# Optimization experiments

Measured on AMD Instinct MI355X. Metric: run time of the kernel, lower is better.

## Reference

```python
import jax, jax.numpy as jnp
import numpy as np

B, N, NH, E = 4, 4096, 16, 64
MD, FF, H, PE = 128, 256, 4, 32
DH = MD // H
SCALE = 1.0 / np.float32(np.sqrt(DH))


def _ln(x, g, b, eps=1e-5):
    m = jnp.mean(x, axis=-1, keepdims=True)
    v = jnp.var(x, axis=-1, keepdims=True)
    return (x - m) * jax.lax.rsqrt(v + eps) * g + b


def setup_inputs() -> dict:
    key = jax.random.key(0)
    ks = jax.random.split(key, 16)
    rn = lambda k, shape: jax.random.normal(k, shape, dtype=jnp.float32) * 0.02
    return {
        "x": jax.random.normal(ks[0], (B, N, NH, E), dtype=jnp.float32),
        "pos1": jax.random.normal(ks[1], (B, N, NH, NH), dtype=jnp.float32),
        "pos2": jax.random.normal(ks[2], (B, N, NH, NH), dtype=jnp.float32),
        # input_mlp: Linear(E->MD, no bias) + LayerNorm
        "W_in": rn(ks[3], (E, MD)), "g_in": jnp.ones((MD,), jnp.float32), "b_in": jnp.zeros((MD,), jnp.float32),
        # pos_embedder (simple MLP on stacked rel-coords) + emb_proj_bias (PE->H, no bias)
        "W_pe": rn(ks[4], (2, PE)),
        "W_bias": rn(ks[5], (PE, H)),
        # MHA qkv projections (with bias) and output projection
        "Wq": rn(ks[6], (MD, MD)), "bq": jnp.zeros((MD,), jnp.float32),
        "Wk": rn(ks[7], (MD, MD)), "bk": jnp.zeros((MD,), jnp.float32),
        "Wv": rn(ks[8], (MD, MD)), "bv": jnp.zeros((MD,), jnp.float32),
        "Wo": rn(ks[9], (MD, MD)), "bo": jnp.zeros((MD,), jnp.float32),
        # mlp_layer: Linear(MD->FF,no bias), SiLU, Linear(FF->MD,no bias)
        "W1": rn(ks[10], (MD, FF)), "W2": rn(ks[11], (FF, MD)),
        "g1": jnp.ones((MD,), jnp.float32), "b1": jnp.zeros((MD,), jnp.float32),
        "g2": jnp.ones((MD,), jnp.float32), "b2": jnp.zeros((MD,), jnp.float32),
    }


def reference(x, pos1, pos2, W_in, g_in, b_in, W_pe, W_bias,
              Wq, bq, Wk, bk, Wv, bv, Wo, bo, W1, W2, g1, b1, g2, b2):
    b, n, nh, _ = x.shape
    # input_mlp
    h = _ln(x @ W_in, g_in, b_in)                      # [b,n,nh,MD]
    t = h.reshape(b * n, nh, MD)                       # windows of nh tokens
    # relative-position bias: pos_embedder then emb_proj_bias
    pe = jax.nn.silu(jnp.stack([pos1, pos2], axis=-1).reshape(b * n, nh, nh, 2) @ W_pe)  # [bn,nh,nh,PE]
    bias = pe @ W_bias                                  # [bn,nh,nh,H]
    # MHA with additive bias
    q = (t @ Wq + bq).reshape(b * n, nh, H, DH)
    k = (t @ Wk + bk).reshape(b * n, nh, H, DH)
    v = (t @ Wv + bv).reshape(b * n, nh, H, DH)
    scores = jnp.einsum('bqhd,bkhd->bhqk', q, k) * SCALE + jnp.transpose(bias, (0, 3, 1, 2))
    att = jax.nn.softmax(scores, axis=-1)               # [bn,H,nh,nh]
    o = jnp.einsum('bhqk,bkhd->bqhd', att, v).reshape(b * n, nh, MD)
    att_out = o @ Wo + bo
    # residual (q_res=True, dropout=0) + norms + FFN
    y = _ln(t + att_out, g1, b1)
    y = _ln(y + jax.nn.silu(y @ W1) @ W2, g2, b2)
    return y.reshape(b, n, nh, MD)
```

## Files before the change

### kernel.cpp

```cpp
#include <hip/hip_runtime.h>
#include <hip/hip_bf16.h>
#include <math.h>

#define NHT 16
#define MD 128
#define FFD 256
#define NHEAD 4
#define DH 32
#define PED 32
#define ED 64
#define SCALE 0.17677669529663687f
#define SCB 136
#define SCU 40

typedef __attribute__((ext_vector_type(8))) short bf8;
typedef __attribute__((ext_vector_type(4))) float f32x4;
union U8 { bf8 v; unsigned short s[8]; uint u[4]; uint4 q; };

#define MFMA __builtin_amdgcn_mfma_f32_16x16x32_bf16

__device__ __forceinline__ unsigned short bf1(float a){
  __hip_bfloat16 h = __float2bfloat16(a);
  return *reinterpret_cast<unsigned short*>(&h);
}
__device__ __forceinline__ float bfh2f(unsigned short s){
  __hip_bfloat16 h = *reinterpret_cast<__hip_bfloat16*>(&s);
  return __bfloat162float(h);
}
__device__ __forceinline__ float silu_f(float x){ return x / (1.f + __expf(-x)); }

__device__ __forceinline__ void lnC(float (&C)[8][4], const float* __restrict__ g,
                                    const float* __restrict__ b, int lm){
#pragma unroll
  for (int r = 0; r < 4; ++r){
    float s = 0.f, ss = 0.f;
#pragma unroll
    for (int nt = 0; nt < 8; ++nt){ s += C[nt][r]; ss = fmaf(C[nt][r], C[nt][r], ss); }
#pragma unroll
    for (int m = 1; m < 16; m <<= 1){ s += __shfl_xor(s, m); ss += __shfl_xor(ss, m); }
    float mean = s * (1.f/128.f);
    float var  = ss * (1.f/128.f) - mean*mean;
    float rs   = rsqrtf(var + 1e-5f);
#pragma unroll
    for (int nt = 0; nt < 8; ++nt)
      C[nt][r] = fmaf((C[nt][r] - mean) * rs, g[nt*16+lm], b[nt*16+lm]);
  }
}

__global__ __launch_bounds__(256)
void packw(const float* __restrict__ Wq, const float* __restrict__ Wk,
           const float* __restrict__ Wv, const float* __restrict__ Wo,
           const float* __restrict__ W1, const float* __restrict__ W2,
           uint4* __restrict__ ws){
  int id = blockIdx.x * 256 + threadIdx.x;
  const float* W; int KT, N, u; uint4* dst;
  if      (id < 2048) { W = Wq;  KT = 4; N = 128; dst = ws;         u = id;         }
  else if (id < 4096) { W = Wk;  KT = 4; N = 128; dst = ws + 2048;  u = id - 2048;  }
  else if (id < 6144) { W = Wv;  KT = 4; N = 128; dst = ws + 4096;  u = id - 4096;  }
  else if (id < 8192) { W = Wo;  KT = 4; N = 128; dst = ws + 6144;  u = id - 6144;  }
  else if (id < 12288){ W = W1;  KT = 4; N = 256; dst = ws + 8192;  u = id - 8192;  }
  else                { W = W2;  KT = 8; N = 128; dst = ws + 12288; u = id - 12288; }
  int lane = u & 63, tile = u >> 6;
  int kt = tile % KT, nt = tile / KT;
  int kr  = kt*32 + ((lane >> 4) << 3);
  int col = nt*16 + (lane & 15);
  const float* p = W + (size_t)kr * N + col;
  U8 hi;
#pragma unroll
  for (int j = 0; j < 8; ++j) hi.s[j] = bf1(p[(size_t)j * N]);
  dst[u] = hi.q;
}

__global__ __launch_bounds__(64)
void nha_mfma(const float* __restrict__ x, const float* __restrict__ pos1,
              const float* __restrict__ pos2,
              const float* __restrict__ W_in,
              const float* __restrict__ g_in, const float* __restrict__ b_in,
              const float* __restrict__ W_pe, const float* __restrict__ W_bias,
              const float* __restrict__ bq, const float* __restrict__ bk,
              const float* __restrict__ bv, const float* __restrict__ bo,
              const float* __restrict__ g1, const float* __restrict__ b1,
              const float* __restrict__ g2, const float* __restrict__ b2,
              const uint4* __restrict__ wsp, float* __restrict__ out)
{
  const uint4* pWq  = wsp;
  const uint4* pWk  = wsp + 2048;
  const uint4* pWv  = wsp + 4096;
  const uint4* pWo  = wsp + 6144;
  const uint4* pW1  = wsp + 8192;
  const uint4* pW2  = wsp + 12288;

  __shared__ __align__(16) unsigned short Qb[NHT*SCB];
  __shared__ __align__(16) unsigned short Kb[NHT*SCB];
  __shared__ __align__(16) unsigned short Vb[NHT*SCB];
  __shared__ __align__(16) unsigned short Tb[NHT*SCB];
  __shared__ __align__(16) unsigned short Ub[NHT*SCU];
  __shared__ __align__(16) float Bsm[NHEAD*NHT*NHT];

  const int tid = threadIdx.x;
  const int wi  = blockIdx.x;
  const int lm  = tid & 15;
  const int lg  = tid >> 4;
  const f32x4 zero4 = {0.f,0.f,0.f,0.f};

  bf8 xA[2];
  {
    const float* xp = x + (size_t)wi*1024 + lm*ED + lg*8;
#pragma unroll
    for (int kt = 0; kt < 2; ++kt){
      U8 h;
#pragma unroll
      for (int j = 0; j < 8; ++j) h.s[j] = bf1(xp[kt*32 + j]);
      xA[kt] = h.v;
    }
  }
  float tC[8][4];
#pragma unroll
  for (int nt = 0; nt < 8; ++nt){
    f32x4 acc = zero4;
#pragma unroll
    for (int kt = 0; kt < 2; ++kt){
      const float* wp = W_in + (size_t)(kt*32 + lg*8)*MD + nt*16 + lm;
      U8 w;
#pragma unroll
      for (int j = 0; j < 8; ++j) w.s[j] = bf1(wp[(size_t)j*MD]);
      acc = MFMA(xA[kt], w.v, acc, 0,0,0);
    }
#pragma unroll
    for (int r = 0; r < 4; ++r) tC[nt][r] = acc[r];
  }
  lnC(tC, g_in, b_in, lm);

#pragma unroll
  for (int nt = 0; nt < 8; ++nt)
#pragma unroll
    for (int r = 0; r < 4; ++r)
      Tb[(lg*4+r)*SCB + nt*16+lm] = bf1(tC[nt][r]);
  __syncthreads();
  bf8 tA[4];
#pragma unroll
  for (int kt = 0; kt < 4; ++kt)
    tA[kt] = *(const bf8*)(Tb + lm*SCB + kt*32 + lg*8);
  __syncthreads();

#pragma unroll
  for (int nt = 0; nt < 8; ++nt){
    float bb = bq[nt*16+lm];
    f32x4 acc = {bb,bb,bb,bb};
#pragma unroll
    for (int kt = 0; kt < 4; ++kt){
      U8 bh; bh.q = pWq[(nt*4+kt)*64 + tid];
      acc = MFMA(tA[kt], bh.v, acc, 0,0,0);
    }
#pragma unroll
    for (int r = 0; r < 4; ++r) Qb[(lg*4+r)*SCB + nt*16+lm] = bf1(acc[r]);
  }
#pragma unroll
  for (int nt = 0; nt < 8; ++nt){
    float bb = bk[nt*16+lm];
    f32x4 acc = {bb,bb,bb,bb};
#pragma unroll
    for (int kt = 0; kt < 4; ++kt){
      U8 bh; bh.q = pWk[(nt*4+kt)*64 + tid];
      acc = MFMA(tA[kt], bh.v, acc, 0,0,0);
    }
#pragma unroll
    for (int r = 0; r < 4; ++r) Kb[(lg*4+r)*SCB + nt*16+lm] = bf1(acc[r]);
  }
#pragma unroll
  for (int nt = 0; nt < 8; ++nt){
    float bb = bv[nt*16+lm];
    f32x4 acc = {bb,bb,bb,bb};
#pragma unroll
    for (int kt = 0; kt < 4; ++kt){
      U8 bh; bh.q = pWv[(nt*4+kt)*64 + tid];
      acc = MFMA(tA[kt], bh.v, acc, 0,0,0);
    }
#pragma unroll
    for (int r = 0; r < 4; ++r) Vb[(lg*4+r)*SCB + nt*16+lm] = bf1(acc[r]);
  }

  for (int p = tid; p < NHT*NHT; p += 64){
    float p1 = pos1[(size_t)wi*256 + p];
    float p2 = pos2[(size_t)wi*256 + p];
    float a0=0.f, a1=0.f, a2=0.f, a3=0.f;
#pragma unroll
    for (int i = 0; i < PED; ++i){
      float e = fmaf(p1, W_pe[i], p2 * W_pe[PED+i]);
      float sv = silu_f(e);
      a0 = fmaf(sv, W_bias[i*4+0], a0);
      a1 = fmaf(sv, W_bias[i*4+1], a1);
      a2 = fmaf(sv, W_bias[i*4+2], a2);
      a3 = fmaf(sv, W_bias[i*4+3], a3);
    }
    Bsm[0*256 + p] = a0; Bsm[1*256 + p] = a1; Bsm[2*256 + p] = a2; Bsm[3*256 + p] = a3;
  }
  __syncthreads();

  {
    const int h  = tid >> 4;
    const int qi = tid & 15;
    float qf[DH];
    {
      const unsigned short* qp = Qb + qi*SCB + h*DH;
#pragma unroll
      for (int d0 = 0; d0 < DH; d0 += 8){
        U8 u; u.v = *(const bf8*)(qp + d0);
#pragma unroll
        for (int j = 0; j < 8; ++j) qf[d0+j] = bfh2f(u.s[j]);
      }
    }
    float sc[NHT];
#pragma unroll
    for (int ki = 0; ki < NHT; ++ki){
      const unsigned short* kp = Kb + ki*SCB + h*DH;
      float dot = 0.f;
#pragma unroll
      for (int d0 = 0; d0 < DH; d0 += 8){
        U8 u; u.v = *(const bf8*)(kp + d0);
#pragma unroll
        for (int j = 0; j < 8; ++j) dot = fmaf(qf[d0+j], bfh2f(u.s[j]), dot);
      }
      sc[ki] = fmaf(dot, SCALE, Bsm[h*256 + qi*16 + ki]);
    }
    float mx = sc[0];
#pragma unroll
    for (int ki = 1; ki < NHT; ++ki) mx = fmaxf(mx, sc[ki]);
    float sum = 0.f;
#pragma unroll
    for (int ki = 0; ki < NHT; ++ki){ sc[ki] = __expf(sc[ki]-mx); sum += sc[ki]; }
    const float inv = 1.f/sum;
    float of[DH];
#pragma unroll
    for (int d = 0; d < DH; ++d) of[d] = 0.f;
#pragma unroll
    for (int ki = 0; ki < NHT; ++ki){
      const unsigned short* vp = Vb + ki*SCB + h*DH;
      const float a = sc[ki];
#pragma unroll
      for (int d0 = 0; d0 < DH; d0 += 8){
        U8 u; u.v = *(const bf8*)(vp + d0);
#pragma unroll
        for (int j = 0; j < 8; ++j) of[d0+j] = fmaf(a, bfh2f(u.s[j]), of[d0+j]);
      }
    }
    unsigned short* op_ = Qb + qi*SCB + h*DH;
#pragma unroll
    for (int d = 0; d < DH; ++d) op_[d] = bf1(of[d]*inv);
  }
  __syncthreads();

  bf8 oA[4];
#pragma unroll
  for (int kt = 0; kt < 4; ++kt)
    oA[kt] = *(const bf8*)(Qb + lm*SCB + kt*32 + lg*8);
#pragma unroll
  for (int nt = 0; nt < 8; ++nt){
    float bb = bo[nt*16+lm];
    f32x4 acc = {bb,bb,bb,bb};
#pragma unroll
    for (int kt = 0; kt < 4; ++kt){
      U8 bh; bh.q = pWo[(nt*4+kt)*64 + tid];
      acc = MFMA(oA[kt], bh.v, acc, 0,0,0);
    }
#pragma unroll
    for (int r = 0; r < 4; ++r) tC[nt][r] += acc[r];
  }
  lnC(tC, g1, b1, lm);
  __syncthreads();

#pragma unroll
  for (int nt = 0; nt < 8; ++nt)
#pragma unroll
    for (int r = 0; r < 4; ++r)
      Tb[(lg*4+r)*SCB + nt*16+lm] = bf1(tC[nt][r]);
  __syncthreads();
  bf8 yA[4];
#pragma unroll
  for (int kt = 0; kt < 4; ++kt)
    yA[kt] = *(const bf8*)(Tb + lm*SCB + kt*32 + lg*8);
  __syncthreads();

  f32x4 acc2[8];
#pragma unroll
  for (int nt = 0; nt < 8; ++nt) acc2[nt] = zero4;
#pragma unroll
  for (int kt2 = 0; kt2 < 8; ++kt2){
#pragma unroll
    for (int sub = 0; sub < 2; ++sub){
      int nt1 = kt2*2 + sub;
      f32x4 a = zero4;
#pragma unroll
      for (int kt = 0; kt < 4; ++kt){
        U8 bh; bh.q = pW1[(nt1*4+kt)*64 + tid];
        a = MFMA(yA[kt], bh.v, a, 0,0,0);
      }
#pragma unroll
      for (int r = 0; r < 4; ++r)
        Ub[(lg*4+r)*SCU + sub*16 + lm] = bf1(silu_f(a[r]));
    }
    __syncthreads();
    bf8 uA = *(const bf8*)(Ub + lm*SCU + lg*8);
    __syncthreads();
#pragma unroll
    for (int nt = 0; nt < 8; ++nt){
      U8 bh; bh.q = pW2[(nt*8+kt2)*64 + tid];
      acc2[nt] = MFMA(uA, bh.v, acc2[nt], 0,0,0);
    }
  }

#pragma unroll
  for (int nt = 0; nt < 8; ++nt)
#pragma unroll
    for (int r = 0; r < 4; ++r) tC[nt][r] += acc2[nt][r];
  lnC(tC, g2, b2, lm);

  float* op = out + (size_t)wi*(NHT*MD);
#pragma unroll
  for (int nt = 0; nt < 8; ++nt)
#pragma unroll
    for (int r = 0; r < 4; ++r)
      op[(lg*4+r)*MD + nt*16+lm] = tC[nt][r];
}

extern "C" void kernel_launch(void* const* d_in, const int* in_sizes, int n_in,
                              void* d_out, int out_size, void* d_ws, size_t ws_size,
                              hipStream_t stream) {
  const float* x     = (const float*)d_in[0];
  const float* pos1  = (const float*)d_in[1];
  const float* pos2  = (const float*)d_in[2];
  const float* W_in  = (const float*)d_in[3];
  const float* g_in  = (const float*)d_in[4];
  const float* b_in  = (const float*)d_in[5];
  const float* W_pe  = (const float*)d_in[6];
  const float* W_bias= (const float*)d_in[7];
  const float* Wq    = (const float*)d_in[8];
  const float* bq    = (const float*)d_in[9];
  const float* Wk    = (const float*)d_in[10];
  const float* bk    = (const float*)d_in[11];
  const float* Wv    = (const float*)d_in[12];
  const float* bv    = (const float*)d_in[13];
  const float* Wo    = (const float*)d_in[14];
  const float* bo    = (const float*)d_in[15];
  const float* W1    = (const float*)d_in[16];
  const float* W2    = (const float*)d_in[17];
  const float* g1    = (const float*)d_in[18];
  const float* b1    = (const float*)d_in[19];
  const float* g2    = (const float*)d_in[20];
  const float* b2    = (const float*)d_in[21];
  float* out = (float*)d_out;
  uint4* ws  = (uint4*)d_ws;

  packw<<<64, 256, 0, stream>>>(Wq, Wk, Wv, Wo, W1, W2, ws);

  const int nwin = in_sizes[0] / (NHT * ED);
  nha_mfma<<<nwin, 64, 0, stream>>>(x, pos1, pos2, W_in, g_in, b_in, W_pe, W_bias,
                                    bq, bk, bv, bo, g1, b1, g2, b2, ws, out);
}
```

Baseline: 452.6 us.

## Prepack W_in to bf16 MFMA layout, keep K/V in fp32 LDS, batch FFN up-projection

Adds a packwin kernel that converts W_in once into the MFMA B-operand layout in workspace, so each window block no longer does strided fp32 global loads plus conversion for W_in. K and V are now stored in LDS as fp32 and read as float4, which removes the bf16 unpack work in the scalar attention loops. The FFN first layer is computed for all 256 hidden units before the second GEMM, which removes the 16 barriers inside the kt2 loop. In exchange, LDS use per block grows a lot (fp32 K/V and a 16x264 Ub buffer), which can reduce how many blocks fit per CU.

```diff
diff --git a/kernel.cpp b/kernel.cpp
--- a/kernel.cpp
+++ b/kernel.cpp
@@ -11,7 +11,8 @@
 #define ED 64
 #define SCALE 0.17677669529663687f
 #define SCB 136
-#define SCU 40
+#define LDT 132
+#define SCUF 264
 
 typedef __attribute__((ext_vector_type(8))) short bf8;
 typedef __attribute__((ext_vector_type(4))) float f32x4;
@@ -71,6 +72,20 @@
   dst[u] = hi.q;
 }
 
+__global__ __launch_bounds__(256)
+void packwin(const float* __restrict__ Win, uint4* __restrict__ ws){
+  int u = blockIdx.x * 256 + threadIdx.x;
+  int lane = u & 63, tile = u >> 6;
+  int kt = tile % 2, nt = tile / 2;
+  int kr  = kt*32 + ((lane >> 4) << 3);
+  int col = nt*16 + (lane & 15);
+  const float* p = Win + (size_t)kr * MD + col;
+  U8 hi;
+#pragma unroll
+  for (int j = 0; j < 8; ++j) hi.s[j] = bf1(p[(size_t)j * MD]);
+  ws[16384 + u] = hi.q;
+}
+
 __global__ __launch_bounds__(64)
 void nha_mfma(const float* __restrict__ x, const float* __restrict__ pos1,
               const float* __restrict__ pos2,
@@ -81,7 +96,7 @@
               const float* __restrict__ bv, const float* __restrict__ bo,
               const float* __restrict__ g1, const float* __restrict__ b1,
               const float* __restrict__ g2, const float* __restrict__ b2,
-              const uint4* __restrict__ wsp, float* __restrict__ out)
+              const uint4* __restrict__ wsp, int useWin, float* __restrict__ out)
 {
   const uint4* pWq  = wsp;
   const uint4* pWk  = wsp + 2048;
@@ -89,12 +104,13 @@
   const uint4* pWo  = wsp + 6144;
   const uint4* pW1  = wsp + 8192;
   const uint4* pW2  = wsp + 12288;
+  const uint4* pWin = wsp + 16384;
 
   __shared__ __align__(16) unsigned short Qb[NHT*SCB];
-  __shared__ __align__(16) unsigned short Kb[NHT*SCB];
-  __shared__ __align__(16) unsigned short Vb[NHT*SCB];
+  __shared__ __align__(16) float Kf[NHT*LDT];
+  __shared__ __align__(16) float Vf[NHT*LDT];
   __shared__ __align__(16) unsigned short Tb[NHT*SCB];
-  __shared__ __align__(16) unsigned short Ub[NHT*SCU];
+  __shared__ __align__(16) unsigned short Ub[NHT*SCUF];
   __shared__ __align__(16) float Bsm[NHEAD*NHT*NHT];
 
   const int tid = threadIdx.x;
@@ -120,10 +136,14 @@
     f32x4 acc = zero4;
 #pragma unroll
     for (int kt = 0; kt < 2; ++kt){
-      const float* wp = W_in + (size_t)(kt*32 + lg*8)*MD + nt*16 + lm;
       U8 w;
-#pragma unroll
-      for (int j = 0; j < 8; ++j) w.s[j] = bf1(wp[(size_t)j*MD]);
+      if (useWin){
+        w.q = pWin[(nt*2+kt)*64 + tid];
+      } else {
+        const float* wp = W_in + (size_t)(kt*32 + lg*8)*MD + nt*16 + lm;
+#pragma unroll
+        for (int j = 0; j < 8; ++j) w.s[j] = bf1(wp[(size_t)j*MD]);
+      }
       acc = MFMA(xA[kt], w.v, acc, 0,0,0);
     }
 #pragma unroll
@@ -165,7 +185,7 @@
       acc = MFMA(tA[kt], bh.v, acc, 0,0,0);
     }
 #pragma unroll
-    for (int r = 0; r < 4; ++r) Kb[(lg*4+r)*SCB + nt*16+lm] = bf1(acc[r]);
+    for (int r = 0; r < 4; ++r) Kf[(lg*4+r)*LDT + nt*16+lm] = acc[r];
   }
 #pragma unroll
   for (int nt = 0; nt < 8; ++nt){
@@ -177,7 +197,7 @@
       acc = MFMA(tA[kt], bh.v, acc, 0,0,0);
     }
 #pragma unroll
-    for (int r = 0; r < 4; ++r) Vb[(lg*4+r)*SCB + nt*16+lm] = bf1(acc[r]);
+    for (int r = 0; r < 4; ++r) Vf[(lg*4+r)*LDT + nt*16+lm] = acc[r];
   }
 
   for (int p = tid; p < NHT*NHT; p += 64){
@@ -213,13 +233,13 @@
     float sc[NHT];
 #pragma unroll
     for (int ki = 0; ki < NHT; ++ki){
-      const unsigned short* kp = Kb + ki*SCB + h*DH;
+      const float* krow = Kf + ki*LDT + h*DH;
       float dot = 0.f;
 #pragma unroll
-      for (int d0 = 0; d0 < DH; d0 += 8){
-        U8 u; u.v = *(const bf8*)(kp + d0);
-#pragma unroll
-        for (int j = 0; j < 8; ++j) dot = fmaf(qf[d0+j], bfh2f(u.s[j]), dot);
+      for (int d = 0; d < DH; d += 4){
+        float4 kv = *(const float4*)(krow + d);
+        dot = fmaf(qf[d], kv.x, dot);   dot = fmaf(qf[d+1], kv.y, dot);
+        dot = fmaf(qf[d+2], kv.z, dot); dot = fmaf(qf[d+3], kv.w, dot);
       }
       sc[ki] = fmaf(dot, SCALE, Bsm[h*256 + qi*16 + ki]);
     }
@@ -235,13 +255,13 @@
     for (int d = 0; d < DH; ++d) of[d] = 0.f;
 #pragma unroll
     for (int ki = 0; ki < NHT; ++ki){
-      const unsigned short* vp = Vb + ki*SCB + h*DH;
+      const float* vrow = Vf + ki*LDT + h*DH;
       const float a = sc[ki];
 #pragma unroll
-      for (int d0 = 0; d0 < DH; d0 += 8){
-        U8 u; u.v = *(const bf8*)(vp + d0);
-#pragma unroll
-        for (int j = 0; j < 8; ++j) of[d0+j] = fmaf(a, bfh2f(u.s[j]), of[d0+j]);
+      for (int d = 0; d < DH; d += 4){
+        float4 vv = *(const float4*)(vrow + d);
+        of[d]   = fmaf(a, vv.x, of[d]);   of[d+1] = fmaf(a, vv.y, of[d+1]);
+        of[d+2] = fmaf(a, vv.z, of[d+2]); of[d+3] = fmaf(a, vv.w, of[d+3]);
       }
     }
     unsigned short* op_ = Qb + qi*SCB + h*DH;
@@ -281,27 +301,25 @@
     yA[kt] = *(const bf8*)(Tb + lm*SCB + kt*32 + lg*8);
   __syncthreads();
 
+#pragma unroll
+  for (int nt1 = 0; nt1 < 16; ++nt1){
+    f32x4 a = zero4;
+#pragma unroll
+    for (int kt = 0; kt < 4; ++kt){
+      U8 bh; bh.q = pW1[(nt1*4+kt)*64 + tid];
+      a = MFMA(yA[kt], bh.v, a, 0,0,0);
+    }
+#pragma unroll
+    for (int r = 0; r < 4; ++r)
+      Ub[(lg*4+r)*SCUF + nt1*16 + lm] = bf1(silu_f(a[r]));
+  }
+  __syncthreads();
   f32x4 acc2[8];
 #pragma unroll
   for (int nt = 0; nt < 8; ++nt) acc2[nt] = zero4;
 #pragma unroll
   for (int kt2 = 0; kt2 < 8; ++kt2){
-#pragma unroll
-    for (int sub = 0; sub < 2; ++sub){
-      int nt1 = kt2*2 + sub;
-      f32x4 a = zero4;
-#pragma unroll
-      for (int kt = 0; kt < 4; ++kt){
-        U8 bh; bh.q = pW1[(nt1*4+kt)*64 + tid];
-        a = MFMA(yA[kt], bh.v, a, 0,0,0);
-      }
-#pragma unroll
-      for (int r = 0; r < 4; ++r)
-        Ub[(lg*4+r)*SCU + sub*16 + lm] = bf1(silu_f(a[r]));
-    }
-    __syncthreads();
-    bf8 uA = *(const bf8*)(Ub + lm*SCU + lg*8);
-    __syncthreads();
+    bf8 uA = *(const bf8*)(Ub + lm*SCUF + kt2*32 + lg*8);
 #pragma unroll
     for (int nt = 0; nt < 8; ++nt){
       U8 bh; bh.q = pW2[(nt*8+kt2)*64 + tid];
@@ -351,9 +369,12 @@
   float* out = (float*)d_out;
   uint4* ws  = (uint4*)d_ws;
 
+  const int useWin = (ws_size >= (size_t)(16384 + 1024) * 16) ? 1 : 0;
+
   packw<<<64, 256, 0, stream>>>(Wq, Wk, Wv, Wo, W1, W2, ws);
+  if (useWin) packwin<<<4, 256, 0, stream>>>(W_in, ws);
 
   const int nwin = in_sizes[0] / (NHT * ED);
   nha_mfma<<<nwin, 64, 0, stream>>>(x, pos1, pos2, W_in, g_in, b_in, W_pe, W_bias,
-                                    bq, bk, bv, bo, g1, b1, g2, b2, ws, out);
-}
+                                    bq, bk, bv, bo, g1, b1, g2, b2, ws, useWin, out);
+}
```

Result: no change. 448.5 us (-0.9%).
